# Optimization experiments

Measured on AMD Instinct MI355X. Metric: run time of the kernel, lower is better.

The kernel has to match this reference:

```python
import jax, jax.numpy as jnp
import numpy as np

H = 12      # num_attention_heads
DM = 768    # hidden_size
HD = DM // H  # head_dim = 64


def setup_inputs() -> dict:
    key = jax.random.key(0)
    ks = jax.random.split(key, 9)
    B, L = 4, 2048
    s = 0.02
    return {
        "hidden_states": jax.random.normal(ks[0], (B, L, DM), jnp.float32),
        "wq": jax.random.normal(ks[1], (DM, DM), jnp.float32) * s,
        "bq": jnp.zeros((DM,), jnp.float32),
        "wk": jax.random.normal(ks[2], (DM, DM), jnp.float32) * s,
        "bk": jnp.zeros((DM,), jnp.float32),
        "wv": jax.random.normal(ks[3], (DM, DM), jnp.float32) * s,
        "bv": jnp.zeros((DM,), jnp.float32),
        "wo": jax.random.normal(ks[4], (DM, DM), jnp.float32) * s,
        "bo": jnp.zeros((DM,), jnp.float32),
    }


def reference(hidden_states, wq, bq, wk, bk, wv, bv, wo, bo):
    B, L, D = hidden_states.shape
    scale = HD ** -0.5
    # torch Linear: x @ W.T + b
    q = hidden_states @ wq.T + bq
    k = hidden_states @ wk.T + bk
    v = hidden_states @ wv.T + bv
    # [B, H, L, HD]
    q = q.reshape(B, L, H, HD).transpose(0, 2, 1, 3)
    k = k.reshape(B, L, H, HD).transpose(0, 2, 1, 3)
    v = v.reshape(B, L, H, HD).transpose(0, 2, 1, 3)
    attn = jnp.einsum('bhqd,bhkd->bhqk', q, k) * scale
    causal = jnp.tril(jnp.ones((L, L), dtype=bool))
    attn = jnp.where(causal, attn, jnp.float32(-jnp.inf))
    attn = jax.nn.softmax(attn, axis=-1)
    out = jnp.einsum('bhqk,bhkd->bhqd', attn, v)
    out = out.transpose(0, 2, 1, 3).reshape(B, L, D)
    return out @ wo.T + bo
```

## Files before the change

kernel.cpp:

```cpp
#include <hip/hip_runtime.h>

typedef unsigned short ushort_t;
typedef __attribute__((ext_vector_type(8))) short short8;
typedef __attribute__((ext_vector_type(4))) float f32x4;

__device__ __forceinline__ ushort_t f2b(float f) {
    union { float f; unsigned int i; } v; v.f = f;
    unsigned int x = v.i;
    return (ushort_t)((x + 0x7fffu + ((x >> 16) & 1u)) >> 16);
}
__device__ __forceinline__ ushort_t f2b_fast(float f) {
    union { float f; unsigned int i; } v; v.f = f;
    return (ushort_t)((v.i + 0x8000u) >> 16);
}
__device__ __forceinline__ float exp2_hw(float x) {
    return __builtin_amdgcn_exp2f(x);
}
__device__ __forceinline__ void dma16(const ushort_t* g, ushort_t* l) {
    __builtin_amdgcn_global_load_lds(
        (const __attribute__((address_space(1))) unsigned int*)g,
        (__attribute__((address_space(3))) unsigned int*)l, 16, 0, 0);
}

__global__ __launch_bounds__(256)
void convert_bf16(const float* __restrict__ hs, const float* __restrict__ wq,
                  const float* __restrict__ wk, const float* __restrict__ wv,
                  const float* __restrict__ wo,
                  ushort_t* __restrict__ hsb, ushort_t* __restrict__ wqb,
                  ushort_t* __restrict__ wkb, ushort_t* __restrict__ wvb,
                  ushort_t* __restrict__ wob)
{
    const int y = blockIdx.y;
    const float* src; ushort_t* dst; int n;
    if (y == 0)      { src = hs; dst = hsb; n = 8192 * 768; }
    else if (y == 1) { src = wq; dst = wqb; n = 768 * 768; }
    else if (y == 2) { src = wk; dst = wkb; n = 768 * 768; }
    else if (y == 3) { src = wv; dst = wvb; n = 768 * 768; }
    else             { src = wo; dst = wob; n = 768 * 768; }
    const int idx = (blockIdx.x * 256 + threadIdx.x) * 8;
    if (idx >= n) return;
    const float4 a = ((const float4*)(src + idx))[0];
    const float4 b = ((const float4*)(src + idx))[1];
    ushort_t tmp[8] = { f2b(a.x), f2b(a.y), f2b(a.z), f2b(a.w),
                        f2b(b.x), f2b(b.y), f2b(b.z), f2b(b.w) };
    *(uint4*)(dst + idx) = *(const uint4*)tmp;
}

#define NIT 24

template<int MODE>
__global__ __launch_bounds__(256, 3)
void gemm_mfma(const ushort_t* __restrict__ A,
               const ushort_t* __restrict__ W0, const ushort_t* __restrict__ W1,
               const ushort_t* __restrict__ W2,
               const float* __restrict__ b0, const float* __restrict__ b1,
               const float* __restrict__ b2,
               void* __restrict__ C0, void* __restrict__ C1, void* __restrict__ C2)
{
    __shared__ __attribute__((aligned(16))) ushort_t Ab[3][128 * 32];
    __shared__ __attribute__((aligned(16))) ushort_t Wb[3][128 * 32];

    const int id   = blockIdx.x;
    const int xcd  = id & 7;
    const int slot = id >> 3;
    int mtile, otile, z;
    if (MODE == 0) {
        mtile = (slot / 18) * 8 + xcd;
        const int rem = slot % 18;
        otile = rem % 6;
        z     = rem / 6;
    } else {
        mtile = (slot / 6) * 8 + xcd;
        otile = slot % 6;
        z     = 0;
    }
    const ushort_t* W = (z == 0) ? W0 : (z == 1) ? W1 : W2;
    const float* bias  = (z == 0) ? b0 : (z == 1) ? b1 : b2;
    void* C            = (z == 0) ? C0 : (z == 1) ? C1 : C2;

    const int t    = threadIdx.x;
    const int lane = t & 63;
    const int w    = t >> 6;
    const int col  = lane & 15;
    const int kg   = lane >> 4;
    const int m0   = mtile * 128;
    const int o0   = otile * 128;
    const int mh   = (w & 1) * 64;
    const int oh   = (w >> 1) * 64;

    f32x4 acc[4][4];
#pragma unroll
    for (int mt = 0; mt < 4; ++mt)
#pragma unroll
        for (int nt = 0; nt < 4; ++nt) acc[mt][nt] = (f32x4){0.f, 0.f, 0.f, 0.f};

    const int lrow = lane >> 2;
    const int lgr  = (lane & 3) ^ ((lane >> 3) & 3);
    const ushort_t* pa = A + (size_t)(m0 + lrow) * 768 + lgr * 8;
    const ushort_t* pw = W + (size_t)(o0 + lrow) * 768 + lgr * 8;

    auto stage = [&](int c, int b) {
#pragma unroll
        for (int j = 0; j < 2; ++j) {
            const int q = 2 * w + j;
            dma16(pa + (size_t)q * (16 * 768) + c * 32, &Ab[b][q * 512]);
            dma16(pw + (size_t)q * (16 * 768) + c * 32, &Wb[b][q * 512]);
        }
    };

    const int gq = (kg ^ ((col >> 1) & 3)) * 8;

    auto step = [&](int it, int cur, int nb) {
        __builtin_amdgcn_s_barrier();
        if (it + 2 < NIT) {
            stage(it + 2, nb);
            asm volatile("s_waitcnt vmcnt(8)" ::: "memory");
        } else if (it + 1 < NIT) {
            asm volatile("s_waitcnt vmcnt(4)" ::: "memory");
        } else {
            asm volatile("s_waitcnt vmcnt(0)" ::: "memory");
        }
        __builtin_amdgcn_sched_barrier(0);

        short8 wf[4], af[4];
#pragma unroll
        for (int nt = 0; nt < 4; ++nt)
            wf[nt] = *(const short8*)&Wb[cur][(oh + nt * 16 + col) * 32 + gq];
#pragma unroll
        for (int mt = 0; mt < 4; ++mt)
            af[mt] = *(const short8*)&Ab[cur][(mh + mt * 16 + col) * 32 + gq];

#pragma unroll
        for (int mt = 0; mt < 4; ++mt)
#pragma unroll
            for (int nt = 0; nt < 4; ++nt)
                acc[mt][nt] = __builtin_amdgcn_mfma_f32_16x16x32_bf16(
                    af[mt], wf[nt], acc[mt][nt], 0, 0, 0);
    };

    stage(0, 0);
    stage(1, 1);
    for (int j = 0; j < NIT; j += 3) {
        step(j + 0, 0, 2);
        step(j + 1, 1, 0);
        step(j + 2, 2, 1);
    }

    float bias_v[4];
#pragma unroll
    for (int nt = 0; nt < 4; ++nt) bias_v[nt] = bias[o0 + oh + nt * 16 + col];
    const float scale = (MODE == 0 && z == 0) ? 0.18033688011112042f : 1.0f;

#pragma unroll
    for (int mt = 0; mt < 4; ++mt)
#pragma unroll
        for (int nt = 0; nt < 4; ++nt) {
            const int mb = m0 + mh + mt * 16 + kg * 4;
            const int o  = o0 + oh + nt * 16 + col;
            if (MODE == 0 && z == 2) {
                ushort_t tmp[4];
#pragma unroll
                for (int r = 0; r < 4; ++r) tmp[r] = f2b(acc[mt][nt][r] + bias_v[nt]);
                const size_t dst = ((size_t)((mb >> 11) * 12 + (o >> 6)) << 17)
                                 + ((size_t)(o & 63) << 11) + (mb & 2047);
                *(uint2*)((ushort_t*)C + dst) = *(const uint2*)tmp;
            } else {
#pragma unroll
                for (int r = 0; r < 4; ++r) {
                    const int m = mb + r;
                    const float v = (acc[mt][nt][r] + bias_v[nt]) * scale;
                    if (MODE == 0) {
                        const size_t dst = ((size_t)((m >> 11) * 12 + (o >> 6)) << 17)
                                         + ((size_t)(m & 2047) << 6) + (o & 63);
                        ((ushort_t*)C)[dst] = f2b(v);
                    } else {
                        ((float*)C)[(size_t)m * 768 + o] = v;
                    }
                }
            }
        }
}

#define KV_STRIDE 72
#define PS_STRIDE 78

__global__ __launch_bounds__(256, 3)
void attn_mfma(const ushort_t* __restrict__ Q, const ushort_t* __restrict__ K,
               const ushort_t* __restrict__ Vt, ushort_t* __restrict__ AO)
{
    __shared__ ushort_t Ks[64 * KV_STRIDE];
    __shared__ ushort_t Vs[64 * KV_STRIDE];
    __shared__ ushort_t Ps[4][16 * PS_STRIDE];

    const int t    = threadIdx.x;
    const int lane = t & 63;
    const int w    = t >> 6;
    const int id   = blockIdx.x;
    const int bh   = ((id >> 3) >> 4) * 8 + (id & 7);
    const int p    = (id >> 3) & 15;
    const size_t base = (size_t)bh << 17;

    const int col = lane & 15;
    const int kg  = lane >> 4;
    const int srow = t >> 2;
    const int scol = (t & 3) << 4;
    const int b = bh / 12, h = bh % 12;

#pragma unroll
    for (int phase = 0; phase < 2; ++phase) {
        const int tile = phase ? p : (31 - p);
        const int q0   = tile << 6;
        const int nch  = tile + 1;

        const ushort_t* pq = Q + base + (size_t)(q0 + 16 * w + col) * 64 + kg * 8;
        const short8 aq0 = *(const short8*)pq;
        const short8 aq1 = *(const short8*)(pq + 32);

        float l_lane[4] = {0.f, 0.f, 0.f, 0.f};
        f32x4 o_acc[4];
#pragma unroll
        for (int vt = 0; vt < 4; ++vt) o_acc[vt] = (f32x4){0.f, 0.f, 0.f, 0.f};

        uint4 ka, kb, va, vb;
        {
            const ushort_t* pk = K  + base + (size_t)srow * 64 + scol;
            const ushort_t* pv = Vt + base + ((size_t)srow << 11) + scol;
            ka = *(const uint4*)pk; kb = *(const uint4*)(pk + 8);
            va = *(const uint4*)pv; vb = *(const uint4*)(pv + 8);
        }

        for (int c = 0; c < nch; ++c) {
            __syncthreads();
            *(uint4*)&Ks[srow * KV_STRIDE + scol]     = ka;
            *(uint4*)&Ks[srow * KV_STRIDE + scol + 8] = kb;
            *(uint4*)&Vs[srow * KV_STRIDE + scol]     = va;
            *(uint4*)&Vs[srow * KV_STRIDE + scol + 8] = vb;
            __syncthreads();

            if (c + 1 < nch) {
                const int k1 = (c + 1) << 6;
                const ushort_t* pk = K  + base + (size_t)(k1 + srow) * 64 + scol;
                const ushort_t* pv = Vt + base + ((size_t)srow << 11) + k1 + scol;
                ka = *(const uint4*)pk; kb = *(const uint4*)(pk + 8);
                va = *(const uint4*)pv; vb = *(const uint4*)(pv + 8);
            }

            f32x4 s[4];
            __builtin_amdgcn_s_setprio(1);
#pragma unroll
            for (int kt = 0; kt < 4; ++kt) {
                const ushort_t* pkf = &Ks[(kt * 16 + col) * KV_STRIDE + kg * 8];
                const short8 b0 = *(const short8*)pkf;
                const short8 b1 = *(const short8*)(pkf + 32);
                f32x4 acc = (f32x4){0.f, 0.f, 0.f, 0.f};
                acc = __builtin_amdgcn_mfma_f32_16x16x32_bf16(aq0, b0, acc, 0, 0, 0);
                acc = __builtin_amdgcn_mfma_f32_16x16x32_bf16(aq1, b1, acc, 0, 0, 0);
                s[kt] = acc;
            }
            __builtin_amdgcn_s_setprio(0);

            const int qrow = q0 + 16 * w + 4 * kg;
            if (c == nch - 1) {
                const int k0 = c << 6;
#pragma unroll
                for (int kt = 0; kt < 4; ++kt)
#pragma unroll
                    for (int r = 0; r < 4; ++r) {
                        const int key = k0 + kt * 16 + col;
                        s[kt][r] = (key > qrow + r) ? 0.f : exp2_hw(s[kt][r]);
                    }
            } else {
#pragma unroll
                for (int kt = 0; kt < 4; ++kt)
#pragma unroll
                    for (int r = 0; r < 4; ++r) s[kt][r] = exp2_hw(s[kt][r]);
            }
#pragma unroll
            for (int r = 0; r < 4; ++r)
                l_lane[r] += (s[0][r] + s[1][r]) + (s[2][r] + s[3][r]);

            ushort_t* ps = Ps[w];
#pragma unroll
            for (int kt = 0; kt < 4; ++kt)
#pragma unroll
                for (int r = 0; r < 4; ++r)
                    ps[(4 * kg + r) * PS_STRIDE + kt * 16 + col] = f2b_fast(s[kt][r]);
            short8 pa0, pa1;
            {
                const ushort_t* pp = ps + (size_t)col * PS_STRIDE + kg * 8;
                pa0 = *(const short8*)pp;
                pa1 = *(const short8*)(pp + 32);
            }

            __builtin_amdgcn_s_setprio(1);
#pragma unroll
            for (int vt = 0; vt < 4; ++vt) {
                const ushort_t* pvf = &Vs[(vt * 16 + col) * KV_STRIDE + kg * 8];
                const short8 v0 = *(const short8*)pvf;
                const short8 v1 = *(const short8*)(pvf + 32);
                f32x4 o = o_acc[vt];
                o = __builtin_amdgcn_mfma_f32_16x16x32_bf16(pa0, v0, o, 0, 0, 0);
                o = __builtin_amdgcn_mfma_f32_16x16x32_bf16(pa1, v1, o, 0, 0, 0);
                o_acc[vt] = o;
            }
            __builtin_amdgcn_s_setprio(0);
        }

        float linv[4];
#pragma unroll
        for (int r = 0; r < 4; ++r) {
            float ls = l_lane[r];
            ls += __shfl_xor(ls, 1);
            ls += __shfl_xor(ls, 2);
            ls += __shfl_xor(ls, 4);
            ls += __shfl_xor(ls, 8);
            linv[r] = 1.f / ls;
        }
#pragma unroll
        for (int vt = 0; vt < 4; ++vt)
#pragma unroll
            for (int r = 0; r < 4; ++r) {
                const int q = q0 + 16 * w + 4 * kg + r;
                AO[((size_t)(b * 2048 + q)) * 768 + h * 64 + vt * 16 + col] =
                    f2b_fast(o_acc[vt][r] * linv[r]);
            }
    }
}

extern "C" void kernel_launch(void* const* d_in, const int* in_sizes, int n_in,
                              void* d_out, int out_size, void* d_ws, size_t ws_size,
                              hipStream_t stream) {
    const float* hs = (const float*)d_in[0];
    const float* wq = (const float*)d_in[1];
    const float* bq = (const float*)d_in[2];
    const float* wk = (const float*)d_in[3];
    const float* bk = (const float*)d_in[4];
    const float* wv = (const float*)d_in[5];
    const float* bv = (const float*)d_in[6];
    const float* wo = (const float*)d_in[7];
    const float* bo = (const float*)d_in[8];
    float* out = (float*)d_out;

    const size_t NB = (size_t)8192 * 768;
    const size_t WN = (size_t)768 * 768;
    ushort_t* hsb = (ushort_t*)d_ws;
    ushort_t* Qb  = hsb + NB;
    ushort_t* Kb  = Qb + NB;
    ushort_t* Vtb = Kb + NB;
    ushort_t* wqb = Vtb + NB;
    ushort_t* wkb = wqb + WN;
    ushort_t* wvb = wkb + WN;
    ushort_t* wob = wvb + WN;
    ushort_t* AO  = hsb;

    dim3 blk(256);
    convert_bf16<<<dim3(3072, 5), blk, 0, stream>>>(hs, wq, wk, wv, wo,
                                                    hsb, wqb, wkb, wvb, wob);
    gemm_mfma<0><<<dim3(1152), blk, 0, stream>>>(hsb, wqb, wkb, wvb,
                                                 bq, bk, bv, Qb, Kb, Vtb);
    attn_mfma<<<dim3(768), blk, 0, stream>>>(Qb, Kb, Vtb, AO);
    gemm_mfma<1><<<dim3(384), blk, 0, stream>>>(AO, wob, wob, wob,
                                                bo, bo, bo, out, out, out);
}
```

Baseline: 227.6 us.

## Stage 128-key K/V blocks per barrier round in causal attention loop

The attention loop now loads 128 keys of K and V into shared memory per round and processes them as two 64-key sub-chunks. This halves the number of __syncthreads barriers and global-to-LDS staging steps per query tile. Each thread prefetches more data into registers. The V tile layout is widened and the P scratch stride is changed from 78 to 76. The costs are more register and LDS pressure, which may hurt occupancy at 3 blocks per CU. When the chunk count is odd, one unused 64-key half is also loaded.

```diff
diff --git a/kernel.cpp b/kernel.cpp
--- a/kernel.cpp
+++ b/kernel.cpp
@@ -181,15 +181,16 @@
         }
 }
 
-#define KV_STRIDE 72
-#define PS_STRIDE 78
+#define KSTR 72
+#define VSTR 136
+#define PS_STRIDE 76
 
 __global__ __launch_bounds__(256, 3)
 void attn_mfma(const ushort_t* __restrict__ Q, const ushort_t* __restrict__ K,
                const ushort_t* __restrict__ Vt, ushort_t* __restrict__ AO)
 {
-    __shared__ ushort_t Ks[64 * KV_STRIDE];
-    __shared__ ushort_t Vs[64 * KV_STRIDE];
+    __shared__ ushort_t Ks[128 * KSTR];
+    __shared__ ushort_t Vs[64 * VSTR];
     __shared__ ushort_t Ps[4][16 * PS_STRIDE];
 
     const int t    = threadIdx.x;
@@ -202,15 +203,19 @@
 
     const int col = lane & 15;
     const int kg  = lane >> 4;
-    const int srow = t >> 2;
-    const int scol = (t & 3) << 4;
     const int b = bh / 12, h = bh % 12;
+
+    const int krow = t >> 1;
+    const int kcol = (t & 1) * 32;
+    const int vrow = t >> 2;
+    const int vcol = (t & 3) * 32;
 
 #pragma unroll
     for (int phase = 0; phase < 2; ++phase) {
         const int tile = phase ? p : (31 - p);
         const int q0   = tile << 6;
         const int nch  = tile + 1;
+        const int nrd  = (nch + 1) >> 1;
 
         const ushort_t* pq = Q + base + (size_t)(q0 + 16 * w + col) * 64 + kg * 8;
         const short8 aq0 = *(const short8*)pq;
@@ -221,35 +226,26 @@
 #pragma unroll
         for (int vt = 0; vt < 4; ++vt) o_acc[vt] = (f32x4){0.f, 0.f, 0.f, 0.f};
 
-        uint4 ka, kb, va, vb;
-        {
-            const ushort_t* pk = K  + base + (size_t)srow * 64 + scol;
-            const ushort_t* pv = Vt + base + ((size_t)srow << 11) + scol;
-            ka = *(const uint4*)pk; kb = *(const uint4*)(pk + 8);
-            va = *(const uint4*)pv; vb = *(const uint4*)(pv + 8);
-        }
-
-        for (int c = 0; c < nch; ++c) {
-            __syncthreads();
-            *(uint4*)&Ks[srow * KV_STRIDE + scol]     = ka;
-            *(uint4*)&Ks[srow * KV_STRIDE + scol + 8] = kb;
-            *(uint4*)&Vs[srow * KV_STRIDE + scol]     = va;
-            *(uint4*)&Vs[srow * KV_STRIDE + scol + 8] = vb;
-            __syncthreads();
-
-            if (c + 1 < nch) {
-                const int k1 = (c + 1) << 6;
-                const ushort_t* pk = K  + base + (size_t)(k1 + srow) * 64 + scol;
-                const ushort_t* pv = Vt + base + ((size_t)srow << 11) + k1 + scol;
-                ka = *(const uint4*)pk; kb = *(const uint4*)(pk + 8);
-                va = *(const uint4*)pv; vb = *(const uint4*)(pv + 8);
-            }
-
+        const int qrow = q0 + 16 * w + 4 * kg;
+
+        uint4 kr[4], vr[4];
+        auto pref = [&](int r) {
+            const ushort_t* pk = K  + base + (size_t)(r * 128 + krow) * 64 + kcol;
+            const ushort_t* pv = Vt + base + ((size_t)vrow << 11) + r * 128 + vcol;
+#pragma unroll
+            for (int j = 0; j < 4; ++j) {
+                kr[j] = *(const uint4*)(pk + j * 8);
+                vr[j] = *(const uint4*)(pv + j * 8);
+            }
+        };
+
+        auto csub = [&](int c, int sub) {
             f32x4 s[4];
             __builtin_amdgcn_s_setprio(1);
 #pragma unroll
             for (int kt = 0; kt < 4; ++kt) {
-                const ushort_t* pkf = &Ks[(kt * 16 + col) * KV_STRIDE + kg * 8];
+                const ushort_t* pkf =
+                    &Ks[(sub * 64 + kt * 16 + col) * KSTR + kg * 8];
                 const short8 b0 = *(const short8*)pkf;
                 const short8 b1 = *(const short8*)(pkf + 32);
                 f32x4 acc = (f32x4){0.f, 0.f, 0.f, 0.f};
@@ -259,7 +255,6 @@
             }
             __builtin_amdgcn_s_setprio(0);
 
-            const int qrow = q0 + 16 * w + 4 * kg;
             if (c == nch - 1) {
                 const int k0 = c << 6;
 #pragma unroll
@@ -295,7 +290,8 @@
             __builtin_amdgcn_s_setprio(1);
 #pragma unroll
             for (int vt = 0; vt < 4; ++vt) {
-                const ushort_t* pvf = &Vs[(vt * 16 + col) * KV_STRIDE + kg * 8];
+                const ushort_t* pvf =
+                    &Vs[(vt * 16 + col) * VSTR + sub * 64 + kg * 8];
                 const short8 v0 = *(const short8*)pvf;
                 const short8 v1 = *(const short8*)(pvf + 32);
                 f32x4 o = o_acc[vt];
@@ -304,6 +300,24 @@
                 o_acc[vt] = o;
             }
             __builtin_amdgcn_s_setprio(0);
+        };
+
+        pref(0);
+
+        for (int r = 0; r < nrd; ++r) {
+            __syncthreads();
+#pragma unroll
+            for (int j = 0; j < 4; ++j) {
+                *(uint4*)&Ks[krow * KSTR + kcol + j * 8] = kr[j];
+                *(uint4*)&Vs[vrow * VSTR + vcol + j * 8] = vr[j];
+            }
+            __syncthreads();
+
+            if (r + 1 < nrd) pref(r + 1);
+
+            const int c0 = 2 * r;
+            csub(c0, 0);
+            if (c0 + 1 < nch) csub(c0 + 1, 1);
         }
 
         float linv[4];
```

Result: slower. 295.8 us (+30.0%).

## Compute transposed S=K·Q^T and shuffle P in registers instead of LDS round-trip

Applied to the files above, without the earlier changes.

The QK^T MFMA now puts keys on the row dimension, so each lane holds scores for a single query column. The probabilities are packed to bf16 with v_cvt_pk_bf16_f32 and rearranged into the PV A-operand layout with cross-lane shuffles and selects, which removes the per-wave Ps LDS buffer and its write/read. This frees LDS and drops a shared-memory round trip per chunk. In exchange it adds shuffle and select instructions, and the row-sum reduction is reworked to match the new layout.

```diff
diff --git a/kernel.cpp b/kernel.cpp
--- a/kernel.cpp
+++ b/kernel.cpp
@@ -182,7 +182,6 @@
 }
 
 #define KV_STRIDE 72
-#define PS_STRIDE 78
 
 __global__ __launch_bounds__(256, 3)
 void attn_mfma(const ushort_t* __restrict__ Q, const ushort_t* __restrict__ K,
@@ -190,7 +189,6 @@
 {
     __shared__ ushort_t Ks[64 * KV_STRIDE];
     __shared__ ushort_t Vs[64 * KV_STRIDE];
-    __shared__ ushort_t Ps[4][16 * PS_STRIDE];
 
     const int t    = threadIdx.x;
     const int lane = t & 63;
@@ -213,10 +211,12 @@
         const int nch  = tile + 1;
 
         const ushort_t* pq = Q + base + (size_t)(q0 + 16 * w + col) * 64 + kg * 8;
-        const short8 aq0 = *(const short8*)pq;
-        const short8 aq1 = *(const short8*)(pq + 32);
-
-        float l_lane[4] = {0.f, 0.f, 0.f, 0.f};
+        const short8 bq0 = *(const short8*)pq;
+        const short8 bq1 = *(const short8*)(pq + 32);
+
+        const int qcur = q0 + 16 * w + col;
+
+        float l_run = 0.f;
         f32x4 o_acc[4];
 #pragma unroll
         for (int vt = 0; vt < 4; ++vt) o_acc[vt] = (f32x4){0.f, 0.f, 0.f, 0.f};
@@ -250,24 +250,23 @@
 #pragma unroll
             for (int kt = 0; kt < 4; ++kt) {
                 const ushort_t* pkf = &Ks[(kt * 16 + col) * KV_STRIDE + kg * 8];
-                const short8 b0 = *(const short8*)pkf;
-                const short8 b1 = *(const short8*)(pkf + 32);
+                const short8 ak0 = *(const short8*)pkf;
+                const short8 ak1 = *(const short8*)(pkf + 32);
                 f32x4 acc = (f32x4){0.f, 0.f, 0.f, 0.f};
-                acc = __builtin_amdgcn_mfma_f32_16x16x32_bf16(aq0, b0, acc, 0, 0, 0);
-                acc = __builtin_amdgcn_mfma_f32_16x16x32_bf16(aq1, b1, acc, 0, 0, 0);
+                acc = __builtin_amdgcn_mfma_f32_16x16x32_bf16(ak0, bq0, acc, 0, 0, 0);
+                acc = __builtin_amdgcn_mfma_f32_16x16x32_bf16(ak1, bq1, acc, 0, 0, 0);
                 s[kt] = acc;
             }
             __builtin_amdgcn_s_setprio(0);
 
-            const int qrow = q0 + 16 * w + 4 * kg;
             if (c == nch - 1) {
                 const int k0 = c << 6;
 #pragma unroll
                 for (int kt = 0; kt < 4; ++kt)
 #pragma unroll
                     for (int r = 0; r < 4; ++r) {
-                        const int key = k0 + kt * 16 + col;
-                        s[kt][r] = (key > qrow + r) ? 0.f : exp2_hw(s[kt][r]);
+                        const int key = k0 + kt * 16 + 4 * kg + r;
+                        s[kt][r] = (key > qcur) ? 0.f : exp2_hw(s[kt][r]);
                     }
             } else {
 #pragma unroll
@@ -276,21 +275,49 @@
                     for (int r = 0; r < 4; ++r) s[kt][r] = exp2_hw(s[kt][r]);
             }
 #pragma unroll
-            for (int r = 0; r < 4; ++r)
-                l_lane[r] += (s[0][r] + s[1][r]) + (s[2][r] + s[3][r]);
-
-            ushort_t* ps = Ps[w];
-#pragma unroll
             for (int kt = 0; kt < 4; ++kt)
-#pragma unroll
-                for (int r = 0; r < 4; ++r)
-                    ps[(4 * kg + r) * PS_STRIDE + kt * 16 + col] = f2b_fast(s[kt][r]);
-            short8 pa0, pa1;
-            {
-                const ushort_t* pp = ps + (size_t)col * PS_STRIDE + kg * 8;
-                pa0 = *(const short8*)pp;
-                pa1 = *(const short8*)(pp + 32);
-            }
+                l_run += (s[kt][0] + s[kt][1]) + (s[kt][2] + s[kt][3]);
+
+            unsigned int P2[4][2];
+#pragma unroll
+            for (int kt = 0; kt < 4; ++kt) {
+                asm("v_cvt_pk_bf16_f32 %0, %1, %2"
+                    : "=v"(P2[kt][0]) : "v"(s[kt][0]), "v"(s[kt][1]));
+                asm("v_cvt_pk_bf16_f32 %0, %1, %2"
+                    : "=v"(P2[kt][1]) : "v"(s[kt][2]), "v"(s[kt][3]));
+            }
+            const bool klo = (kg < 2);
+            unsigned int X16[4], X32[4];
+            X16[0] = klo ? P2[0][0] : P2[1][0];
+            X16[1] = klo ? P2[0][1] : P2[1][1];
+            X16[2] = klo ? P2[2][0] : P2[3][0];
+            X16[3] = klo ? P2[2][1] : P2[3][1];
+            X32[0] = klo ? P2[1][0] : P2[0][0];
+            X32[1] = klo ? P2[1][1] : P2[0][1];
+            X32[2] = klo ? P2[3][0] : P2[2][0];
+            X32[3] = klo ? P2[3][1] : P2[2][1];
+            unsigned int R16[4], R32[4], R48[4];
+#pragma unroll
+            for (int j = 0; j < 4; ++j) {
+                R16[j] = (unsigned int)__shfl_xor((int)X16[j], 16);
+                R32[j] = (unsigned int)__shfl_xor((int)X32[j], 32);
+                R48[j] = (unsigned int)__shfl_xor((int)X32[j], 48);
+            }
+            unsigned int Fv[4], Sv[4];
+#pragma unroll
+            for (int j = 0; j < 4; ++j) {
+                const unsigned int flo = (kg == 0) ? X16[j] : R48[j];
+                const unsigned int fhi = (kg == 2) ? R32[j] : R16[j];
+                Fv[j] = klo ? flo : fhi;
+                const unsigned int slo = (kg == 0) ? R16[j] : R32[j];
+                const unsigned int shi = (kg == 2) ? R48[j] : X16[j];
+                Sv[j] = klo ? slo : shi;
+            }
+            union { unsigned int u[4]; short8 v; } A0, A1;
+            A0.u[0] = Fv[0]; A0.u[1] = Fv[1]; A0.u[2] = Sv[0]; A0.u[3] = Sv[1];
+            A1.u[0] = Fv[2]; A1.u[1] = Fv[3]; A1.u[2] = Sv[2]; A1.u[3] = Sv[3];
+            const short8 pa0 = A0.v;
+            const short8 pa1 = A1.v;
 
             __builtin_amdgcn_s_setprio(1);
 #pragma unroll
@@ -306,23 +333,21 @@
             __builtin_amdgcn_s_setprio(0);
         }
 
-        float linv[4];
-#pragma unroll
-        for (int r = 0; r < 4; ++r) {
-            float ls = l_lane[r];
-            ls += __shfl_xor(ls, 1);
-            ls += __shfl_xor(ls, 2);
-            ls += __shfl_xor(ls, 4);
-            ls += __shfl_xor(ls, 8);
-            linv[r] = 1.f / ls;
-        }
+        float ls = l_run;
+        ls += __shfl_xor(ls, 16);
+        ls += __shfl_xor(ls, 32);
+        const float linv = 1.f / ls;
+        float linv4[4];
+#pragma unroll
+        for (int r = 0; r < 4; ++r)
+            linv4[r] = __shfl(linv, 4 * kg + r);
 #pragma unroll
         for (int vt = 0; vt < 4; ++vt)
 #pragma unroll
             for (int r = 0; r < 4; ++r) {
                 const int q = q0 + 16 * w + 4 * kg + r;
                 AO[((size_t)(b * 2048 + q)) * 768 + h * 64 + vt * 16 + col] =
-                    f2b_fast(o_acc[vt][r] * linv[r]);
+                    f2b_fast(o_acc[vt][r] * linv4[r]);
             }
     }
 }
```

Measured after the change: 208.9 us. 8.2% less time.
